# Kernel optimization log

Hardware: AMD Instinct MI355X
Metric: run time of the kernel (lower is better)

The kernel has to match this reference:

```python
import jax, jax.numpy as jnp
import numpy as np

N_NODES = 50000
N_FEAT = 256
N_HID = 32
N_HEADS = 8
N_CLASSES = 32
N_EDGES = 800000
NEG_SLOPE = 0.2  # PyG GATConv default leaky_relu slope


def setup_inputs() -> dict:
    key = jax.random.key(0)
    ks = jax.random.split(key, 10)
    x = jax.random.normal(ks[0], (N_NODES, N_FEAT), dtype=jnp.float32)
    edge_index = jax.random.randint(ks[1], (2, N_EDGES), 0, N_NODES, dtype=jnp.int64)
    s1 = 1.0 / np.sqrt(N_FEAT)
    s2 = 1.0 / np.sqrt(N_HID * N_HEADS)
    W1 = jax.random.normal(ks[2], (N_FEAT, N_HEADS * N_HID), dtype=jnp.float32) * s1
    a_src1 = jax.random.normal(ks[3], (N_HEADS, N_HID), dtype=jnp.float32) * s1
    a_dst1 = jax.random.normal(ks[4], (N_HEADS, N_HID), dtype=jnp.float32) * s1
    b1 = jnp.zeros((N_HEADS * N_HID,), dtype=jnp.float32)
    W2 = jax.random.normal(ks[5], (N_HEADS * N_HID, N_CLASSES), dtype=jnp.float32) * s2
    a_src2 = jax.random.normal(ks[6], (1, N_CLASSES), dtype=jnp.float32) * s2
    a_dst2 = jax.random.normal(ks[7], (1, N_CLASSES), dtype=jnp.float32) * s2
    b2 = jnp.zeros((N_CLASSES,), dtype=jnp.float32)
    return {"x": x, "edge_index": edge_index, "W1": W1, "a_src1": a_src1,
            "a_dst1": a_dst1, "b1": b1, "W2": W2, "a_src2": a_src2,
            "a_dst2": a_dst2, "b2": b2}


def _gat_conv(h, src, dst, n_nodes, W, a_src, a_dst, heads, ch):
    # h: [N, F_in]; returns [N, heads, ch] aggregated per-node features
    z = (h @ W).reshape(n_nodes, heads, ch)           # [N,H,C]
    alpha_src = jnp.einsum('nhc,hc->nh', z, a_src)    # [N,H]
    alpha_dst = jnp.einsum('nhc,hc->nh', z, a_dst)    # [N,H]
    logits = jax.nn.leaky_relu(alpha_src[src] + alpha_dst[dst], NEG_SLOPE)  # [E,H]
    # segment softmax over incoming edges of each dst node
    m = jax.ops.segment_max(logits, dst, num_segments=n_nodes)  # [N,H]
    e = jnp.exp(logits - m[dst])                                 # [E,H]
    denom = jax.ops.segment_sum(e, dst, num_segments=n_nodes)   # [N,H]
    alpha = e / denom[dst]                                       # [E,H]
    msg = z[src] * alpha[:, :, None]                             # [E,H,C]
    return jax.ops.segment_sum(msg, dst, num_segments=n_nodes)  # [N,H,C]


def reference(x, edge_index, W1, a_src1, a_dst1, b1, W2, a_src2, a_dst2, b2):
    n = x.shape[0]
    # PyG GATConv default: add self loops
    loops = jnp.arange(n, dtype=edge_index.dtype)
    src = jnp.concatenate([edge_index[0], loops])
    dst = jnp.concatenate([edge_index[1], loops])
    h1 = _gat_conv(x, src, dst, n, W1, a_src1, a_dst1, N_HEADS, N_HID)
    h1 = h1.reshape(n, N_HEADS * N_HID) + b1          # concat=True
    h1 = jax.nn.elu(h1)
    # dropout is a no-op in eval mode
    h2 = _gat_conv(h1, src, dst, n, W2, a_src2, a_dst2, 1, N_CLASSES)
    out = h2.mean(axis=1) + b2                        # concat=False, heads=1
    return out
```

## Files before the change

kernel.cpp:

```cpp
#include <hip/hip_runtime.h>

#define NNODES 50000
#define NFEAT 256
#define NHID 32
#define NHEADS 8
#define NCLASSES 32
#define NEDGES 800000
#define ETOT (NEDGES + NNODES)
#define NSCAN_BLK 196
#define GEMM1_BLKS 782
#define SCAT_BLKS 3321

typedef __attribute__((ext_vector_type(8))) short short8;
typedef __attribute__((ext_vector_type(4))) float f32x4;

__device__ __forceinline__ void get_edge(const int* __restrict__ ei, int e,
                                         int& s, int& d) {
    if (e < NEDGES) { s = ei[e]; d = ei[NEDGES + e]; }
    else            { s = e - NEDGES; d = s; }
}
__device__ __forceinline__ float lrelu(float x) { return x > 0.f ? x : 0.2f * x; }
__device__ __forceinline__ unsigned short f2bf(float f) {
    unsigned u = __float_as_uint(f);
    unsigned r = u + 0x7fffu + ((u >> 16) & 1u);
    return (unsigned short)(r >> 16);
}
__device__ __forceinline__ float bflo(unsigned u) { return __uint_as_float(u << 16); }
__device__ __forceinline__ float bfhi(unsigned u) { return __uint_as_float(u & 0xffff0000u); }

__global__ void wprep_hist_k(const float* __restrict__ W1, const float* __restrict__ W2,
                             short8* __restrict__ W1frag, short8* __restrict__ W2frag,
                             const int* __restrict__ ei, int* __restrict__ deg) {
    if (blockIdx.x < 36) {
        int idx = blockIdx.x * 256 + threadIdx.x;
        if (idx < 8192) {
            int kc = idx >> 10, r = idx & 1023;
            int nt = r >> 6, lane = r & 63;
            int l16 = lane & 15, quad = lane >> 4;
            int n = nt * 16 + l16, k0 = kc * 32 + quad * 8;
            short8 v;
#pragma unroll
            for (int j = 0; j < 8; ++j) v[j] = (short)f2bf(W1[(k0 + j) * 256 + n]);
            W1frag[idx] = v;
        } else if (idx < 8192 + 1024) {
            int g = idx - 8192;
            int kc = g >> 7, r = g & 127;
            int nt = r >> 6, lane = r & 63;
            int l16 = lane & 15, quad = lane >> 4;
            int n = nt * 16 + l16, k0 = kc * 32 + quad * 8;
            short8 v;
#pragma unroll
            for (int j = 0; j < 8; ++j) v[j] = (short)f2bf(W2[(k0 + j) * 32 + n]);
            W2frag[g] = v;
        }
    } else {
        int e = (blockIdx.x - 36) * 256 + threadIdx.x;
        if (e >= ETOT) return;
        int s, d;
        get_edge(ei, e, s, d);
        atomicAdd(&deg[d], 1);
    }
}

__global__ void scan_part_k(const int* __restrict__ deg, int* __restrict__ row_local,
                            int* __restrict__ bsum) {
    __shared__ int ws[4];
    int t = threadIdx.x, lane = t & 63, wid = t >> 6;
    int idx = blockIdx.x * 256 + t;
    int v = (idx < NNODES) ? deg[idx] : 0;
    int inc = v;
#pragma unroll
    for (int off = 1; off < 64; off <<= 1) {
        int u = __shfl_up(inc, off, 64);
        if (lane >= off) inc += u;
    }
    if (lane == 63) ws[wid] = inc;
    __syncthreads();
    int woff = 0;
#pragma unroll
    for (int j = 0; j < 4; ++j) woff += (j < wid) ? ws[j] : 0;
    if (idx < NNODES) row_local[idx] = woff + inc - v;
    if (t == 255) bsum[blockIdx.x] = woff + inc;
}

__global__ void scan_fix_k(const int* __restrict__ row_local, const int* __restrict__ bsum,
                           int* __restrict__ row_start) {
    __shared__ int ws[4];
    __shared__ int sboff;
    int t = threadIdx.x, lane = t & 63, wid = t >> 6;
    int v = (t < NSCAN_BLK) ? bsum[t] : 0;
    int inc = v;
#pragma unroll
    for (int off = 1; off < 64; off <<= 1) {
        int u = __shfl_up(inc, off, 64);
        if (lane >= off) inc += u;
    }
    if (lane == 63) ws[wid] = inc;
    __syncthreads();
    int woff = 0;
#pragma unroll
    for (int j = 0; j < 4; ++j) woff += (j < wid) ? ws[j] : 0;
    if (t == blockIdx.x) sboff = woff + inc - v;
    __syncthreads();
    int idx = blockIdx.x * 256 + t;
    if (idx < NNODES) row_start[idx] = row_local[idx] + sboff;
    if (idx == 0) row_start[NNODES] = ETOT;
}

__global__ __launch_bounds__(256) void gemm1_scatter_k(
        const float* __restrict__ x, const short8* __restrict__ Wfrag,
        const float* __restrict__ av, const float* __restrict__ bv,
        unsigned short* __restrict__ z1, float* __restrict__ as_, float* __restrict__ ad_,
        const int* __restrict__ ei, const int* __restrict__ row_start,
        int* __restrict__ cursor, int* __restrict__ csr_src) {
    if (blockIdx.x >= GEMM1_BLKS) {
        int e = (blockIdx.x - GEMM1_BLKS) * 256 + threadIdx.x;
        if (e >= ETOT) return;
        int s, d;
        get_edge(ei, e, s, d);
        int pos = atomicAdd(&cursor[d], 1);
        csr_src[row_start[d] + pos] = s;
        return;
    }
    int t = threadIdx.x;
    int w = t >> 6, lane = t & 63;
    int quad = lane >> 4, l16 = lane & 15;
    int mA = blockIdx.x * 64 + w * 16 + l16;
    int mAl = min(mA, NNODES - 1);

    f32x4 acc[16];
#pragma unroll
    for (int nt = 0; nt < 16; ++nt) acc[nt] = (f32x4){0.f, 0.f, 0.f, 0.f};

#pragma unroll 2
    for (int kc = 0; kc < 8; ++kc) {
        int k0 = kc * 32 + quad * 8;
        const float4* xp = (const float4*)(x + (size_t)mAl * 256 + k0);
        float4 a0 = xp[0], a1 = xp[1];
        short8 af;
        af[0] = (short)f2bf(a0.x); af[1] = (short)f2bf(a0.y);
        af[2] = (short)f2bf(a0.z); af[3] = (short)f2bf(a0.w);
        af[4] = (short)f2bf(a1.x); af[5] = (short)f2bf(a1.y);
        af[6] = (short)f2bf(a1.z); af[7] = (short)f2bf(a1.w);
        short8 bfr[16];
#pragma unroll
        for (int nt = 0; nt < 16; ++nt) bfr[nt] = Wfrag[kc * 1024 + nt * 64 + lane];
#pragma unroll
        for (int nt = 0; nt < 16; ++nt)
            acc[nt] = __builtin_amdgcn_mfma_f32_16x16x32_bf16(af, bfr[nt], acc[nt], 0, 0, 0);
    }
    int mrow0 = blockIdx.x * 64 + w * 16 + quad * 4;
#pragma unroll
    for (int nt = 0; nt < 16; ++nt) {
        int n = nt * 16 + l16;
#pragma unroll
        for (int r = 0; r < 4; ++r) {
            int mr = mrow0 + r;
            if (mr < NNODES) z1[(size_t)mr * 256 + n] = f2bf(acc[nt][r]);
        }
    }
#pragma unroll
    for (int h = 0; h < 8; ++h) {
        float av0 = av[(2 * h) * 16 + l16], av1v = av[(2 * h + 1) * 16 + l16];
        float bv0 = bv[(2 * h) * 16 + l16], bv1v = bv[(2 * h + 1) * 16 + l16];
#pragma unroll
        for (int r = 0; r < 4; ++r) {
            float pa = acc[2 * h][r] * av0 + acc[2 * h + 1][r] * av1v;
            float pb = acc[2 * h][r] * bv0 + acc[2 * h + 1][r] * bv1v;
#pragma unroll
            for (int off = 1; off < 16; off <<= 1) {
                pa += __shfl_xor(pa, off, 64);
                pb += __shfl_xor(pb, off, 64);
            }
            int mr = mrow0 + r;
            if (l16 == 0 && mr < NNODES) { as_[mr * 8 + h] = pa; ad_[mr * 8 + h] = pb; }
        }
    }
}

__global__ __launch_bounds__(256) void gemm2_mfma_k(
        const unsigned short* __restrict__ h1, const short8* __restrict__ Wfrag,
        const float* __restrict__ av, const float* __restrict__ bv,
        unsigned short* __restrict__ z2b, float* __restrict__ as_, float* __restrict__ ad_) {
    int w = threadIdx.x >> 6, lane = threadIdx.x & 63;
    int quad = lane >> 4, l16 = lane & 15;
    int mA = blockIdx.x * 64 + w * 16 + l16;
    int mAl = min(mA, NNODES - 1);

    f32x4 acc[2];
    acc[0] = (f32x4){0.f, 0.f, 0.f, 0.f};
    acc[1] = (f32x4){0.f, 0.f, 0.f, 0.f};
    for (int kc = 0; kc < 8; ++kc) {
        int k0 = kc * 32 + quad * 8;
        short8 af = *(const short8*)(h1 + (size_t)mAl * 256 + k0);
#pragma unroll
        for (int nt = 0; nt < 2; ++nt) {
            short8 bf8 = Wfrag[kc * 128 + nt * 64 + lane];
            acc[nt] = __builtin_amdgcn_mfma_f32_16x16x32_bf16(af, bf8, acc[nt], 0, 0, 0);
        }
    }
    int mrow0 = blockIdx.x * 64 + w * 16 + quad * 4;
    float av0 = av[l16], av1v = av[16 + l16];
    float bv0 = bv[l16], bv1v = bv[16 + l16];
#pragma unroll
    for (int r = 0; r < 4; ++r) {
        int mr = mrow0 + r;
        float pa = acc[0][r] * av0 + acc[1][r] * av1v;
        float pb = acc[0][r] * bv0 + acc[1][r] * bv1v;
#pragma unroll
        for (int off = 1; off < 16; off <<= 1) {
            pa += __shfl_xor(pa, off, 64);
            pb += __shfl_xor(pb, off, 64);
        }
        if (mr < NNODES) {
            z2b[(size_t)mr * 32 + l16] = f2bf(acc[0][r]);
            z2b[(size_t)mr * 32 + 16 + l16] = f2bf(acc[1][r]);
            if (l16 == 0) { as_[mr] = pa; ad_[mr] = pb; }
        }
    }
}

__global__ void agg1_csr_k(const int* __restrict__ row_start, const int* __restrict__ csr_src,
                           const unsigned short* __restrict__ z, const float* __restrict__ as_,
                           const float* __restrict__ ad_, const float* __restrict__ b,
                           unsigned short* __restrict__ h1) {
    int wv = threadIdx.x >> 6, lane = threadIdx.x & 63;
    int d = blockIdx.x * 4 + wv;
    int h = lane >> 3;
    int c0 = lane * 4;
    int e8 = lane & 7;
    float adh = ad_[d * 8 + h];
    int beg = row_start[d], end = row_start[d + 1];
    float sum = 0.f, a0 = 0.f, a1 = 0.f, a2 = 0.f, a3 = 0.f;
    int i = beg;
    for (; i + 8 <= end; i += 8) {
        int sv = csr_src[i + e8];
        float myw = __expf(lrelu(as_[sv * 8 + h] + adh));
        int se[8];
        float we[8];
#pragma unroll
        for (int e = 0; e < 8; ++e) {
            se[e] = __shfl(sv, e, 64);
            we[e] = __shfl(myw, (lane & 56) | e, 64);
        }
        uint2 q[8];
#pragma unroll
        for (int e = 0; e < 8; ++e)
            q[e] = *(const uint2*)(z + (size_t)se[e] * 256 + c0);
#pragma unroll
        for (int e = 0; e < 8; ++e) {
            float wgt = we[e];
            sum += wgt;
            a0 += wgt * bflo(q[e].x);
            a1 += wgt * bfhi(q[e].x);
            a2 += wgt * bflo(q[e].y);
            a3 += wgt * bfhi(q[e].y);
        }
    }
    for (; i < end; ++i) {
        int s = csr_src[i];
        float wgt = __expf(lrelu(as_[s * 8 + h] + adh));
        uint2 zz = *(const uint2*)(z + (size_t)s * 256 + c0);
        sum += wgt;
        a0 += wgt * bflo(zz.x);
        a1 += wgt * bfhi(zz.x);
        a2 += wgt * bflo(zz.y);
        a3 += wgt * bfhi(zz.y);
    }
    float inv = 1.f / sum;
    float o0 = a0 * inv + b[c0 + 0];
    float o1 = a1 * inv + b[c0 + 1];
    float o2 = a2 * inv + b[c0 + 2];
    float o3 = a3 * inv + b[c0 + 3];
    o0 = o0 > 0.f ? o0 : expm1f(o0);
    o1 = o1 > 0.f ? o1 : expm1f(o1);
    o2 = o2 > 0.f ? o2 : expm1f(o2);
    o3 = o3 > 0.f ? o3 : expm1f(o3);
    uint2 pk;
    pk.x = (unsigned)f2bf(o0) | ((unsigned)f2bf(o1) << 16);
    pk.y = (unsigned)f2bf(o2) | ((unsigned)f2bf(o3) << 16);
    *(uint2*)(h1 + (size_t)d * 256 + c0) = pk;
}

__global__ void agg2_csr_k(const int* __restrict__ row_start, const int* __restrict__ csr_src,
                           const unsigned short* __restrict__ z2b, const float* __restrict__ as_,
                           const float* __restrict__ ad_, const float* __restrict__ b,
                           float* __restrict__ out) {
    int g = blockIdx.x * 16 + (threadIdx.x >> 4);
    int l = threadIdx.x & 15;
    int lane = threadIdx.x & 63;
    int c0 = l * 2;
    int beg = row_start[g], end = row_start[g + 1];
    float adn = ad_[g];
    int e8 = l & 7;
    int gb = lane & 48;
    float sum = 0.f, a0 = 0.f, a1 = 0.f;
    int i = beg;
    for (; i + 8 <= end; i += 8) {
        int sv = csr_src[i + e8];
        float myw = __expf(lrelu(as_[sv] + adn));
        int se[8];
        float we[8];
#pragma unroll
        for (int e = 0; e < 8; ++e) {
            se[e] = __shfl(sv, gb | e, 64);
            we[e] = __shfl(myw, gb | (8 | e), 64);
        }
        unsigned q[8];
#pragma unroll
        for (int e = 0; e < 8; ++e)
            q[e] = *(const unsigned*)(z2b + (size_t)se[e] * 32 + c0);
#pragma unroll
        for (int e = 0; e < 8; ++e) {
            float wgt = we[e];
            sum += wgt;
            a0 += wgt * bflo(q[e]);
            a1 += wgt * bfhi(q[e]);
        }
    }
    for (; i < end; ++i) {
        int s = csr_src[i];
        float wgt = __expf(lrelu(as_[s] + adn));
        unsigned q = *(const unsigned*)(z2b + (size_t)s * 32 + c0);
        sum += wgt;
        a0 += wgt * bflo(q);
        a1 += wgt * bfhi(q);
    }
    float inv = 1.f / sum;
    float2 o;
    o.x = a0 * inv + b[c0];
    o.y = a1 * inv + b[c0 + 1];
    *(float2*)(out + (size_t)g * 32 + c0) = o;
}

extern "C" void kernel_launch(void* const* d_in, const int* in_sizes, int n_in,
                              void* d_out, int out_size, void* d_ws, size_t ws_size,
                              hipStream_t stream) {
    const float* x   = (const float*)d_in[0];
    const int*   ei  = (const int*)d_in[1];
    const float* W1  = (const float*)d_in[2];
    const float* av1 = (const float*)d_in[3];
    const float* bv1 = (const float*)d_in[4];
    const float* b1  = (const float*)d_in[5];
    const float* W2  = (const float*)d_in[6];
    const float* av2 = (const float*)d_in[7];
    const float* bv2 = (const float*)d_in[8];
    const float* b2  = (const float*)d_in[9];
    float* out = (float*)d_out;

    unsigned short* z1 = (unsigned short*)d_ws;
    unsigned short* h1 = (unsigned short*)((float*)d_ws + 6400000);
    float* as1 = (float*)d_ws + 12800000;
    float* ad1 = as1 + 400000;
    unsigned short* z2b = (unsigned short*)(ad1 + 400000);
    float* as2 = ad1 + 400000 + 800000;
    float* ad2 = as2 + 50000;
    short8* W1frag = (short8*)(ad2 + 50000);
    short8* W2frag = W1frag + 8192;
    int* deg       = (int*)(ad2 + 50000) + 36864;
    int* cursor    = deg + 50000;
    int* row_start = cursor + 50000;
    int* csr_src   = row_start + 50001;
    int* row_local = csr_src + 850000;
    int* bsum      = row_local + 50000;

    hipMemsetAsync(deg, 0, (size_t)100000 * 4, stream);

    wprep_hist_k<<<36 + SCAT_BLKS, 256, 0, stream>>>(W1, W2, W1frag, W2frag, ei, deg);
    scan_part_k<<<NSCAN_BLK, 256, 0, stream>>>(deg, row_local, bsum);
    scan_fix_k<<<NSCAN_BLK, 256, 0, stream>>>(row_local, bsum, row_start);

    gemm1_scatter_k<<<GEMM1_BLKS + SCAT_BLKS, 256, 0, stream>>>(
        x, W1frag, av1, bv1, z1, as1, ad1, ei, row_start, cursor, csr_src);
    agg1_csr_k<<<(NNODES + 3) / 4, 256, 0, stream>>>(row_start, csr_src, z1, as1, ad1, b1, h1);

    gemm2_mfma_k<<<(NNODES + 63) / 64, 256, 0, stream>>>(h1, W2frag, av2, bv2, z2b, as2, ad2);
    agg2_csr_k<<<NNODES / 16, 256, 0, stream>>>(row_start, csr_src, z2b, as2, ad2, b2, out);
}
```

Before: 300.5 us.

## Pre-convert x to bf16 in prep kernel and reuse histogram atomics for CSR positions

Adds a block range to the prep kernel that converts x from fp32 to bf16 once into a scratch buffer, so the GEMM1 kernel loads packed bf16 fragments instead of fp32 plus per-lane conversion. The degree histogram now records the atomicAdd return value per edge (epos), which lets the CSR scatter write directly without a second atomic pass or a cursor array, and halves the memset. The cost is an extra full write and read of x in bf16 (about 25 MB of traffic) and an 850k-int epos buffer.

```diff
diff --git a/kernel.cpp b/kernel.cpp
--- a/kernel.cpp
+++ b/kernel.cpp
@@ -10,6 +10,7 @@
 #define NSCAN_BLK 196
 #define GEMM1_BLKS 782
 #define SCAT_BLKS 3321
+#define XCONV_BLKS 6250
 
 typedef __attribute__((ext_vector_type(8))) short short8;
 typedef __attribute__((ext_vector_type(4))) float f32x4;
@@ -28,11 +29,14 @@
 __device__ __forceinline__ float bflo(unsigned u) { return __uint_as_float(u << 16); }
 __device__ __forceinline__ float bfhi(unsigned u) { return __uint_as_float(u & 0xffff0000u); }
 
-__global__ void wprep_hist_k(const float* __restrict__ W1, const float* __restrict__ W2,
-                             short8* __restrict__ W1frag, short8* __restrict__ W2frag,
-                             const int* __restrict__ ei, int* __restrict__ deg) {
-    if (blockIdx.x < 36) {
-        int idx = blockIdx.x * 256 + threadIdx.x;
+__global__ void prep_k(const float* __restrict__ W1, const float* __restrict__ W2,
+                       short8* __restrict__ W1frag, short8* __restrict__ W2frag,
+                       const float* __restrict__ x, short8* __restrict__ xb,
+                       const int* __restrict__ ei, int* __restrict__ deg,
+                       int* __restrict__ epos) {
+    int b = blockIdx.x;
+    if (b < 36) {
+        int idx = b * 256 + threadIdx.x;
         if (idx < 8192) {
             int kc = idx >> 10, r = idx & 1023;
             int nt = r >> 6, lane = r & 63;
@@ -53,12 +57,22 @@
             for (int j = 0; j < 8; ++j) v[j] = (short)f2bf(W2[(k0 + j) * 32 + n]);
             W2frag[g] = v;
         }
+    } else if (b < 36 + XCONV_BLKS) {
+        int i = (b - 36) * 256 + threadIdx.x;
+        const float4* xp = (const float4*)x + (size_t)i * 2;
+        float4 a0 = xp[0], a1 = xp[1];
+        short8 v;
+        v[0] = (short)f2bf(a0.x); v[1] = (short)f2bf(a0.y);
+        v[2] = (short)f2bf(a0.z); v[3] = (short)f2bf(a0.w);
+        v[4] = (short)f2bf(a1.x); v[5] = (short)f2bf(a1.y);
+        v[6] = (short)f2bf(a1.z); v[7] = (short)f2bf(a1.w);
+        xb[i] = v;
     } else {
-        int e = (blockIdx.x - 36) * 256 + threadIdx.x;
+        int e = (b - 36 - XCONV_BLKS) * 256 + threadIdx.x;
         if (e >= ETOT) return;
         int s, d;
         get_edge(ei, e, s, d);
-        atomicAdd(&deg[d], 1);
+        epos[e] = atomicAdd(&deg[d], 1);
     }
 }
 
@@ -108,18 +122,17 @@
 }
 
 __global__ __launch_bounds__(256) void gemm1_scatter_k(
-        const float* __restrict__ x, const short8* __restrict__ Wfrag,
+        const short8* __restrict__ xb, const short8* __restrict__ Wfrag,
         const float* __restrict__ av, const float* __restrict__ bv,
         unsigned short* __restrict__ z1, float* __restrict__ as_, float* __restrict__ ad_,
         const int* __restrict__ ei, const int* __restrict__ row_start,
-        int* __restrict__ cursor, int* __restrict__ csr_src) {
+        const int* __restrict__ epos, int* __restrict__ csr_src) {
     if (blockIdx.x >= GEMM1_BLKS) {
         int e = (blockIdx.x - GEMM1_BLKS) * 256 + threadIdx.x;
         if (e >= ETOT) return;
         int s, d;
         get_edge(ei, e, s, d);
-        int pos = atomicAdd(&cursor[d], 1);
-        csr_src[row_start[d] + pos] = s;
+        csr_src[row_start[d] + epos[e]] = s;
         return;
     }
     int t = threadIdx.x;
@@ -134,14 +147,7 @@
 
 #pragma unroll 2
     for (int kc = 0; kc < 8; ++kc) {
-        int k0 = kc * 32 + quad * 8;
-        const float4* xp = (const float4*)(x + (size_t)mAl * 256 + k0);
-        float4 a0 = xp[0], a1 = xp[1];
-        short8 af;
-        af[0] = (short)f2bf(a0.x); af[1] = (short)f2bf(a0.y);
-        af[2] = (short)f2bf(a0.z); af[3] = (short)f2bf(a0.w);
-        af[4] = (short)f2bf(a1.x); af[5] = (short)f2bf(a1.y);
-        af[6] = (short)f2bf(a1.z); af[7] = (short)f2bf(a1.w);
+        short8 af = xb[(size_t)mAl * 32 + kc * 4 + quad];
         short8 bfr[16];
 #pragma unroll
         for (int nt = 0; nt < 16; ++nt) bfr[nt] = Wfrag[kc * 1024 + nt * 64 + lane];
@@ -350,6 +356,7 @@
 
     unsigned short* z1 = (unsigned short*)d_ws;
     unsigned short* h1 = (unsigned short*)((float*)d_ws + 6400000);
+    short8* xb = (short8*)h1;
     float* as1 = (float*)d_ws + 12800000;
     float* ad1 = as1 + 400000;
     unsigned short* z2b = (unsigned short*)(ad1 + 400000);
@@ -357,21 +364,22 @@
     float* ad2 = as2 + 50000;
     short8* W1frag = (short8*)(ad2 + 50000);
     short8* W2frag = W1frag + 8192;
-    int* deg       = (int*)(ad2 + 50000) + 36864;
-    int* cursor    = deg + 50000;
-    int* row_start = cursor + 50000;
+    int* row_start = (int*)(ad2 + 50000) + 36864;
     int* csr_src   = row_start + 50001;
-    int* row_local = csr_src + 850000;
-    int* bsum      = row_local + 50000;
-
-    hipMemsetAsync(deg, 0, (size_t)100000 * 4, stream);
-
-    wprep_hist_k<<<36 + SCAT_BLKS, 256, 0, stream>>>(W1, W2, W1frag, W2frag, ei, deg);
+    int* bsum      = csr_src + 850000;
+    int* deg       = bsum + 256;
+    int* epos      = deg + 50000;
+    int* row_local = epos + 850000;
+
+    hipMemsetAsync(deg, 0, (size_t)50000 * 4, stream);
+
+    prep_k<<<36 + XCONV_BLKS + SCAT_BLKS, 256, 0, stream>>>(
+        W1, W2, W1frag, W2frag, x, xb, ei, deg, epos);
     scan_part_k<<<NSCAN_BLK, 256, 0, stream>>>(deg, row_local, bsum);
     scan_fix_k<<<NSCAN_BLK, 256, 0, stream>>>(row_local, bsum, row_start);
 
     gemm1_scatter_k<<<GEMM1_BLKS + SCAT_BLKS, 256, 0, stream>>>(
-        x, W1frag, av1, bv1, z1, as1, ad1, ei, row_start, cursor, csr_src);
+        xb, W1frag, av1, bv1, z1, as1, ad1, ei, row_start, epos, csr_src);
     agg1_csr_k<<<(NNODES + 3) / 4, 256, 0, stream>>>(row_start, csr_src, z1, as1, ad1, b1, h1);
 
     gemm2_mfma_k<<<(NNODES + 63) / 64, 256, 0, stream>>>(h1, W2frag, av2, bv2, z2b, as2, ad2);
```

Measured after the change: 300.9 us. Within noise of the previous version (+0.1%).
